# Performance work log

Measured on AMD Instinct MI355X. Metric: run time of the kernel, lower is better.

The kernel has to match this reference:

```python
import jax, jax.numpy as jnp
import numpy as np

MODES = 32
WIDTH = 64
FACTOR = 2
N_LAYERS = 4


def dct_matrix(N):
    # Ortho DCT-II matrix D: dct(x) along last axis = x @ D.T ; idct(y) = y @ D
    n = jnp.arange(N, dtype=jnp.float32)
    k = n[:, None]
    D = jnp.cos(jnp.pi * (n[None, :] + 0.5) * k / N) * jnp.sqrt(2.0 / N)
    D = D.at[0].mul(1.0 / jnp.sqrt(2.0))
    return D


def setup_inputs() -> dict:
    key = jax.random.key(0)
    ks = jax.random.split(key, 16)
    B, M, N, IN_DIM = 4, 256, 256, 12
    hid = WIDTH * FACTOR
    xav_f = jnp.sqrt(2.0 / (WIDTH + WIDTH))  # xavier_normal for (in,out,modes)
    inp = {
        'x': jax.random.normal(ks[0], (B, M, N, IN_DIM), jnp.float32),
        'W_in': jax.random.normal(ks[1], (WIDTH, IN_DIM), jnp.float32) * (1.0 / jnp.sqrt(IN_DIM)),
        'b_in': jnp.zeros((WIDTH,), jnp.float32),
        'fw0': jax.random.normal(ks[2], (N_LAYERS, WIDTH, WIDTH, MODES), jnp.float32) * xav_f,
        'fw1': jax.random.normal(ks[3], (N_LAYERS, WIDTH, WIDTH, MODES), jnp.float32) * xav_f,
        'ffW1': jax.random.normal(ks[4], (N_LAYERS, hid, WIDTH), jnp.float32) * (1.0 / jnp.sqrt(WIDTH)),
        'ffb1': jnp.zeros((N_LAYERS, hid), jnp.float32),
        'ffW2': jax.random.normal(ks[5], (N_LAYERS, WIDTH, hid), jnp.float32) * (1.0 / jnp.sqrt(hid)),
        'ffb2': jnp.zeros((N_LAYERS, WIDTH), jnp.float32),
        'W_o1': jax.random.normal(ks[6], (128, WIDTH), jnp.float32) * (1.0 / jnp.sqrt(WIDTH)),
        'b_o1': jnp.zeros((128,), jnp.float32),
        'W_o2': jax.random.normal(ks[7], (1, 128), jnp.float32) * (1.0 / jnp.sqrt(128.0)),
        'b_o2': jnp.zeros((1,), jnp.float32),
    }
    return inp


def forward_fourier(x, w0, w1, DM, DN):
    # x: [B, M, N, I] channels-last -> [B, I, M, N]
    x = jnp.transpose(x, (0, 3, 1, 2))
    # --- y direction: DCT along N, truncated mode mix, IDCT ---
    x_fty = jnp.einsum('bimn,kn->bimk', x, DN)            # dct, [B,I,M,N]
    xy_m = jnp.einsum('bixy,ioy->boxy', x_fty[..., :MODES], w0)  # [B,O,M,modes]
    xy = jnp.einsum('boxy,yn->boxn', xy_m, DN[:MODES, :])        # idct of zero-padded spectrum
    # --- x direction: DCT along M ---
    x2 = jnp.swapaxes(x, -1, -2)                          # [B,I,N,M]
    x_ftx = jnp.einsum('binm,km->bink', x2, DM)
    xx_m = jnp.einsum('bixy,ioy->boxy', x_ftx[..., :MODES], w1)  # [B,O,N,modes]
    xx = jnp.einsum('boxy,ym->boxm', xx_m, DM[:MODES, :])        # [B,O,N,M]
    xx = jnp.swapaxes(xx, -1, -2)                         # [B,O,M,N]
    out = xx + xy
    return jnp.transpose(out, (0, 2, 3, 1))               # [B,M,N,O]


def feed_forward(h, W1, b1, W2, b2):
    h = jax.nn.relu(h @ W1.T + b1)
    return h @ W2.T + b2


def reference(x, W_in, b_in, fw0, fw1, ffW1, ffb1, ffW2, ffb2, W_o1, b_o1, W_o2, b_o2):
    B, M, N, _ = x.shape
    DM = dct_matrix(M)
    DN = dct_matrix(N)
    x = x @ W_in.T + b_in                                  # in_proj, [B,M,N,width]
    b = x
    for i in range(N_LAYERS):
        h = forward_fourier(x, fw0[i], fw1[i], DM, DN)
        b = feed_forward(h, ffW1[i], ffb1[i], ffW2[i], ffb2[i])
        x = x + b
    # use_fork=False: out applied to the LAST backcast b
    o = jax.nn.relu(b @ W_o1.T + b_o1) * 0 + (b @ W_o1.T + b_o1)  # WNLinear has no activation
    o = b @ W_o1.T + b_o1
    forecast = o @ W_o2.T + b_o2                           # [B,M,N,1]
    return forecast
```

## Files before the change

### kernel.cpp

```cpp
#include <hip/hip_runtime.h>
#include <hip/hip_bf16.h>
#include <math.h>

#define BATCH 4
#define MMDIM 256
#define NNDIM 256
#define CH 64
#define NMODES 32
#define HID 128
#define NLAYERS 4
#define XPLANE 16777216L

typedef __attribute__((ext_vector_type(8))) short bfrag;
typedef __attribute__((ext_vector_type(8))) ushort u16x8;
typedef __attribute__((ext_vector_type(4))) float f32x4;

__device__ inline ushort f2bf(float x) {
    union { float f; uint u; } v; v.f = x;
    uint r = v.u + 0x7fff + ((v.u >> 16) & 1);
    return (ushort)(r >> 16);
}
__device__ inline float bf2f(ushort h) {
    union { uint u; float f; } v; v.u = (uint)h << 16; return v.f;
}
__device__ inline void split(float v, ushort& hi, ushort& lo) {
    __hip_bfloat16 h = __float2bfloat16(v);
    hi = __builtin_bit_cast(ushort, h);
    lo = __builtin_bit_cast(ushort, __float2bfloat16(v - __bfloat162float(h)));
}
#define MFMA __builtin_amdgcn_mfma_f32_16x16x32_bf16


__global__ __launch_bounds__(256) void k_build_T(float* __restrict__ T) {
    int k = blockIdx.x, n = threadIdx.x;
    double v = cos(M_PI * (n + 0.5) * (double)k / 256.0) * sqrt(2.0 / 256.0);
    if (k == 0) v *= 0.7071067811865476;
    T[k * 256 + n] = (float)v;
}

__global__ __launch_bounds__(256) void k_wt(const float* __restrict__ fw, float* __restrict__ wt) {
    int idx = blockIdx.x * 256 + threadIdx.x;
    int l = idx >> 17, r = idx & 131071;
    int y = r >> 12, i = (r >> 6) & 63, o = r & 63;
    wt[idx] = fw[((l * 64 + i) * 64 + o) * 32 + y];
}

__global__ __launch_bounds__(256) void k_Tfrag(const float* __restrict__ T, ushort* __restrict__ Tf) {
    int idx = blockIdx.x * 256 + threadIdx.x;
    int j = idx & 7, lane = (idx >> 3) & 63, ks = (idx >> 9) & 7, yt = idx >> 12;
    float v = T[(yt * 16 + (lane & 15)) * 256 + ks * 32 + ((lane >> 4) << 3) + j];
    ushort hh = f2bf(v);
    Tf[idx] = hh; Tf[idx + 8192] = f2bf(v - bf2f(hh));
}

__global__ __launch_bounds__(256) void k_Ttfrag(const float* __restrict__ T, ushort* __restrict__ Ttf) {
    int idx = blockIdx.x * 256 + threadIdx.x;
    int j = idx & 7, lane = (idx >> 3) & 63, at = idx >> 9;
    float v = T[(((lane >> 4) << 3) + j) * 256 + at * 16 + (lane & 15)];
    ushort hh = f2bf(v);
    Ttf[idx] = hh; Ttf[idx + 8192] = f2bf(v - bf2f(hh));
}

__global__ __launch_bounds__(256) void k_wfrag(const float* __restrict__ W,
                                               ushort* __restrict__ hi, ushort* __restrict__ lo,
                                               int N, int K) {
    int idx = blockIdx.x * 256 + threadIdx.x;
    int per_l = N * K;
    int l = idx / per_l, r = idx % per_l;
    int jj = r & 7, lane = (r >> 3) & 63;
    int ks = (r >> 9) % (K >> 5);
    int nt = r / (512 * (K >> 5));
    int row = nt * 16 + (lane & 15);
    int col = ks * 32 + ((lane >> 4) << 3) + jj;
    float v = W[(long)l * per_l + row * K + col];
    ushort h = f2bf(v);
    hi[idx] = h;
    lo[idx] = f2bf(v - bf2f(h));
}

__global__ void k_head(const float* __restrict__ W_o1, const float* __restrict__ b_o1,
                       const float* __restrict__ W_o2, const float* __restrict__ b_o2,
                       float* __restrict__ Weff, float* __restrict__ beff) {
    int c = threadIdx.x;
    float acc = 0.f;
    for (int j = 0; j < 128; j++) acc += W_o2[j] * W_o1[j * 64 + c];
    Weff[c] = acc;
    if (c == 0) {
        float bb = 0.f;
        for (int j = 0; j < 128; j++) bb += W_o2[j] * b_o1[j];
        beff[0] = bb + b_o2[0];
    }
}

__global__ __launch_bounds__(256) void k_inproj_bf(const float* __restrict__ xin,
                                                   const float* __restrict__ W_in,
                                                   const float* __restrict__ b_in,
                                                   ushort* __restrict__ xbf) {
    __shared__ __align__(16) ushort tile[2][64][72];
    int t = threadIdx.x;
    int bid = blockIdx.x;
    int b = bid >> 10, m = (bid >> 2) & 255, n0 = (bid & 3) * 64;
    int c = t & 63, ng = t >> 6;
    long pbase = (long)(b * 256 + m) * 256 + n0;
    float w[12];
#pragma unroll
    for (int d = 0; d < 12; d++) w[d] = W_in[c * 12 + d];
    float bc = b_in[c];
#pragma unroll 4
    for (int i = 0; i < 16; i++) {
        int nl = ng * 16 + i;
        const float* xr = xin + (pbase + nl) * 12;
        float acc = bc;
#pragma unroll
        for (int d = 0; d < 12; d++) acc += xr[d] * w[d];
        ushort hh, ll;
        split(acc, hh, ll);
        tile[0][c][nl] = hh;
        tile[1][c][nl] = ll;
    }
    __syncthreads();
    int c2 = t >> 2, ch = t & 3;
#pragma unroll
    for (int pl = 0; pl < 2; pl++) {
        const ushort* s = &tile[pl][c2][ch * 16];
        u16x8 v0 = *(const u16x8*)s;
        u16x8 v1 = *(const u16x8*)(s + 8);
        ushort* dst = xbf + (long)pl * XPLANE + ((long)(b * 256 + m) * 64 + c2) * 256 + n0 + ch * 16;
        *(u16x8*)dst = v0; *(u16x8*)(dst + 8) = v1;
    }
}

__global__ __launch_bounds__(256) void k_tx(const ushort* __restrict__ src, ushort* __restrict__ dst) {
    __shared__ __align__(16) ushort tl[64][72];
    int t = threadIdx.x;
    int bid = blockIdx.x;
    int ntile = bid & 3, mt = (bid >> 2) & 3, c = (bid >> 4) & 63, b = (bid >> 10) & 3, pl = bid >> 12;
    int m0 = mt * 64, n0 = ntile * 64;
    const ushort* sp = src + (long)pl * XPLANE;
    ushort* dp = dst + (long)pl * XPLANE;
    {
        int row = t >> 2, ch = (t & 3) * 16;
        const ushort* p = sp + ((long)(b * 256 + m0 + row) * 64 + c) * 256 + n0 + ch;
        u16x8 v0 = *(const u16x8*)p;
        u16x8 v1 = *(const u16x8*)(p + 8);
#pragma unroll
        for (int k = 0; k < 8; k++) tl[ch + k][row] = v0[k];
#pragma unroll
        for (int k = 0; k < 8; k++) tl[ch + 8 + k][row] = v1[k];
    }
    __syncthreads();
    {
        int nrow = t >> 2, mch = (t & 3) * 16;
        const ushort* s = &tl[nrow][mch];
        u16x8 v0 = *(const u16x8*)s;
        u16x8 v1 = *(const u16x8*)(s + 8);
        ushort* p = dp + ((long)(b * 256 + n0 + nrow) * 64 + c) * 256 + m0 + mch;
        *(u16x8*)p = v0; *(u16x8*)(p + 8) = v1;
    }
}

__global__ __launch_bounds__(256) void k_spec(const ushort* __restrict__ xbf,
                                              const ushort* __restrict__ Tf,
                                              const ushort* __restrict__ Ttf,
                                              const float* __restrict__ wt,
                                              float* __restrict__ hdst,
                                              long strideA, long strideF, int accum) {
    __shared__ float Xs[32][68];
    __shared__ __align__(16) ushort Xmb[2][64][40];
    int t = threadIdx.x;
    int lane = t & 63, wv = t >> 6, l15 = lane & 15, l4 = lane >> 4;
    int bf = blockIdx.x;
    const ushort* xb = xbf + (long)bf * 16384;

    f32x4 a0 = {0.f, 0.f, 0.f, 0.f}, a1 = {0.f, 0.f, 0.f, 0.f};
    int c0 = wv * 16;
#pragma unroll
    for (int ks = 0; ks < 8; ks++) {
        const ushort* bp = xb + (c0 + l15) * 256 + ks * 32 + l4 * 8;
        bfrag bhi = *(const bfrag*)bp;
        bfrag blo = *(const bfrag*)(bp + XPLANE);
        const ushort* ap0 = Tf + (long)((0 * 8 + ks) * 64 + lane) * 8;
        const ushort* ap1 = Tf + (long)((1 * 8 + ks) * 64 + lane) * 8;
        bfrag a0h = *(const bfrag*)ap0, a0l = *(const bfrag*)(ap0 + 8192);
        bfrag a1h = *(const bfrag*)ap1, a1l = *(const bfrag*)(ap1 + 8192);
        a0 = MFMA(a0h, bhi, a0, 0, 0, 0);
        a0 = MFMA(a0h, blo, a0, 0, 0, 0);
        a0 = MFMA(a0l, bhi, a0, 0, 0, 0);
        a1 = MFMA(a1h, bhi, a1, 0, 0, 0);
        a1 = MFMA(a1h, blo, a1, 0, 0, 0);
        a1 = MFMA(a1l, bhi, a1, 0, 0, 0);
    }
#pragma unroll
    for (int r = 0; r < 4; r++) {
        Xs[l4 * 4 + r][c0 + l15] = a0[r];
        Xs[16 + l4 * 4 + r][c0 + l15] = a1[r];
    }
    __syncthreads();

    {
        int og = t & 15, yq = t >> 4;
#pragma unroll
        for (int yy = 0; yy < 2; yy++) {
            int y = yq * 2 + yy;
            const float* wb = wt + (long)y * 4096 + og * 4;
            f32x4 a = {0.f, 0.f, 0.f, 0.f};
#pragma unroll 8
            for (int i = 0; i < 64; i++) {
                float xv = Xs[y][i];
                float4 wv = *(const float4*)(wb + i * 64);
                a.x += xv * wv.x; a.y += xv * wv.y; a.z += xv * wv.z; a.w += xv * wv.w;
            }
#pragma unroll
            for (int e = 0; e < 4; e++) {
                ushort hh, ll;
                split(a[e], hh, ll);
                Xmb[0][og * 4 + e][y] = hh;
                Xmb[1][og * 4 + e][y] = ll;
            }
        }
    }
    __syncthreads();

    bfrag vbh[4], vbl[4];
#pragma unroll
    for (int ot = 0; ot < 4; ot++) {
        vbh[ot] = *(const bfrag*)(&Xmb[0][ot * 16 + l15][l4 * 8]);
        vbl[ot] = *(const bfrag*)(&Xmb[1][ot * 16 + l15][l4 * 8]);
    }
    int b = bf >> 8, f = bf & 255;
    float* hb = hdst + (long)b * 4194304 + (long)f * strideF;
#pragma unroll
    for (int ai = 0; ai < 4; ai++) {
        int at = wv * 4 + ai;
        const ushort* ap = Ttf + (long)(at * 64 + lane) * 8;
        bfrag th = *(const bfrag*)ap, tl_ = *(const bfrag*)(ap + 8192);
#pragma unroll
        for (int ot = 0; ot < 4; ot++) {
            f32x4 acc = {0.f, 0.f, 0.f, 0.f};
            acc = MFMA(th, vbh[ot], acc, 0, 0, 0);
            acc = MFMA(th, vbl[ot], acc, 0, 0, 0);
            acc = MFMA(tl_, vbh[ot], acc, 0, 0, 0);
            int arow = at * 16 + l4 * 4;
            float* op = hb + (long)arow * strideA + ot * 16 + l15;
            if (accum) {
#pragma unroll
                for (int r = 0; r < 4; r++) op[(long)r * strideA] += acc[r];
            } else {
#pragma unroll
                for (int r = 0; r < 4; r++) op[(long)r * strideA] = acc[r];
            }
        }
    }
}

#define ASW 136
__global__ __launch_bounds__(256) void k_ff(const float* __restrict__ h,
                                            ushort* __restrict__ xbfw,
                                            const ushort* __restrict__ W1hi, const ushort* __restrict__ W1lo,
                                            const float* __restrict__ b1,
                                            const ushort* __restrict__ W2hi, const ushort* __restrict__ W2lo,
                                            const float* __restrict__ b2,
                                            const float* __restrict__ Weff, const float* __restrict__ beff,
                                            float* __restrict__ out, int last) {
    __shared__ __align__(16) ushort Asb[2][64][ASW];
    int t = threadIdx.x;
    int lane = t & 63, wv = t >> 6;
    int l15 = lane & 15, l4 = lane >> 4;
    long p0 = (long)blockIdx.x * 64;

    f32x4 acc1[8];
#pragma unroll
    for (int nt = 0; nt < 8; nt++) acc1[nt] = (f32x4){0.f, 0.f, 0.f, 0.f};
#pragma unroll
    for (int ks = 0; ks < 2; ks++) {
        const float* hp = h + (p0 + wv * 16 + l15) * 64 + ks * 32 + l4 * 8;
        float4 h0 = *(const float4*)hp;
        float4 h1 = *(const float4*)(hp + 4);
        bfrag ahi, alo;
#pragma unroll
        for (int j = 0; j < 8; j++) {
            float v = (j < 4) ? (&h0.x)[j] : (&h1.x)[j - 4];
            ushort hh, ll;
            split(v, hh, ll);
            ahi[j] = (short)hh; alo[j] = (short)ll;
        }
#pragma unroll
        for (int nt = 0; nt < 8; nt++) {
            long off = (long)((nt * 2 + ks) * 64 + lane) * 8;
            bfrag bhi = *(const bfrag*)(W1hi + off);
            bfrag blo = *(const bfrag*)(W1lo + off);
            acc1[nt] = MFMA(ahi, bhi, acc1[nt], 0, 0, 0);
            acc1[nt] = MFMA(ahi, blo, acc1[nt], 0, 0, 0);
            acc1[nt] = MFMA(alo, bhi, acc1[nt], 0, 0, 0);
        }
    }
#pragma unroll
    for (int nt = 0; nt < 8; nt++) {
        float bj = b1[nt * 16 + l15];
        int j = nt * 16 + l15;
#pragma unroll
        for (int r = 0; r < 4; r++) {
            float v = fmaxf(acc1[nt][r] + bj, 0.f);
            int px = wv * 16 + l4 * 4 + r;
            ushort hh, ll;
            split(v, hh, ll);
            Asb[0][px][j] = hh;
            Asb[1][px][j] = ll;
        }
    }
    __syncthreads();

    f32x4 acc2[4];
#pragma unroll
    for (int nt = 0; nt < 4; nt++) acc2[nt] = (f32x4){0.f, 0.f, 0.f, 0.f};
#pragma unroll
    for (int ks = 0; ks < 4; ks++) {
        bfrag ahi = *(const bfrag*)(&Asb[0][wv * 16 + l15][ks * 32 + l4 * 8]);
        bfrag alo = *(const bfrag*)(&Asb[1][wv * 16 + l15][ks * 32 + l4 * 8]);
#pragma unroll
        for (int nt = 0; nt < 4; nt++) {
            long off = (long)((nt * 4 + ks) * 64 + lane) * 8;
            bfrag bhi = *(const bfrag*)(W2hi + off);
            bfrag blo = *(const bfrag*)(W2lo + off);
            acc2[nt] = MFMA(ahi, bhi, acc2[nt], 0, 0, 0);
            acc2[nt] = MFMA(ahi, blo, acc2[nt], 0, 0, 0);
            acc2[nt] = MFMA(alo, bhi, acc2[nt], 0, 0, 0);
        }
    }

    if (last) {
        float be = beff[0];
#pragma unroll
        for (int r = 0; r < 4; r++) {
            float v = 0.f;
#pragma unroll
            for (int nt = 0; nt < 4; nt++) {
                int c = nt * 16 + l15;
                v += (acc2[nt][r] + b2[c]) * Weff[c];
            }
            v += __shfl_xor(v, 1, 64);
            v += __shfl_xor(v, 2, 64);
            v += __shfl_xor(v, 4, 64);
            v += __shfl_xor(v, 8, 64);
            if (l15 == 0) out[p0 + wv * 16 + l4 * 4 + r] = v + be;
        }
    } else {
        __syncthreads();
        ushort* tile = &Asb[0][0][0];
        int b = (int)(p0 >> 16), m = (int)((p0 >> 8) & 255), n0 = (int)(p0 & 255);
        int c2 = t >> 2, ch = t & 3;
#pragma unroll
        for (int pl = 0; pl < 2; pl++) {
            const ushort* src = xbfw + (long)pl * XPLANE + ((long)(b * 256 + m) * 64 + c2) * 256 + n0 + ch * 16;
            u16x8 v0 = *(const u16x8*)src;
            u16x8 v1 = *(const u16x8*)(src + 8);
            ushort* d = tile + (pl * 64 + c2) * 72 + ch * 16;
            *(u16x8*)d = v0; *(u16x8*)(d + 8) = v1;
        }
        __syncthreads();
#pragma unroll
        for (int nt = 0; nt < 4; nt++) {
            int c = nt * 16 + l15;
            float bc = b2[c];
#pragma unroll
            for (int r = 0; r < 4; r++) {
                int nl = wv * 16 + l4 * 4 + r;
                float res = bf2f(tile[(0 * 64 + c) * 72 + nl]) + bf2f(tile[(1 * 64 + c) * 72 + nl]);
                float v = res + acc2[nt][r] + bc;
                ushort hh, ll;
                split(v, hh, ll);
                tile[(0 * 64 + c) * 72 + nl] = hh;
                tile[(1 * 64 + c) * 72 + nl] = ll;
            }
        }
        __syncthreads();
#pragma unroll
        for (int pl = 0; pl < 2; pl++) {
            const ushort* s = tile + (pl * 64 + c2) * 72 + ch * 16;
            u16x8 v0 = *(const u16x8*)s;
            u16x8 v1 = *(const u16x8*)(s + 8);
            ushort* dst = xbfw + (long)pl * XPLANE + ((long)(b * 256 + m) * 64 + c2) * 256 + n0 + ch * 16;
            *(u16x8*)dst = v0; *(u16x8*)(dst + 8) = v1;
        }
    }
}


extern "C" void kernel_launch(void* const* d_in, const int* in_sizes, int n_in,
                              void* d_out, int out_size, void* d_ws, size_t ws_size,
                              hipStream_t stream) {
    const float* x_in = (const float*)d_in[0];
    const float* W_in = (const float*)d_in[1];
    const float* b_in = (const float*)d_in[2];
    const float* fw0  = (const float*)d_in[3];
    const float* fw1  = (const float*)d_in[4];
    const float* ffW1 = (const float*)d_in[5];
    const float* ffb1 = (const float*)d_in[6];
    const float* ffW2 = (const float*)d_in[7];
    const float* ffb2 = (const float*)d_in[8];
    const float* W_o1 = (const float*)d_in[9];
    const float* b_o1 = (const float*)d_in[10];
    const float* W_o2 = (const float*)d_in[11];
    const float* b_o2 = (const float*)d_in[12];
    float* out = (float*)d_out;

    float* ws   = (float*)d_ws;
    float* T    = ws;
    float* w0t  = T + 8192;
    float* w1t  = w0t + 524288;
    float* Weff = w1t + 524288;
    float* beff = Weff + 64;
    float* h    = beff + 64;
    ushort* Tfrag  = (ushort*)(h + 16777216);
    ushort* Ttfrag = Tfrag + 16384;
    ushort* W1f_hi = Ttfrag + 16384;
    ushort* W1f_lo = W1f_hi + 32768;
    ushort* W2f_hi = W1f_lo + 32768;
    ushort* W2f_lo = W2f_hi + 32768;
    ushort* xbf_y  = W2f_lo + 32768;
    ushort* xbf_x  = xbf_y + 2 * XPLANE;

    k_build_T<<<32, 256, 0, stream>>>(T);
    k_wt<<<2048, 256, 0, stream>>>(fw0, w0t);
    k_wt<<<2048, 256, 0, stream>>>(fw1, w1t);
    k_Tfrag<<<32, 256, 0, stream>>>(T, Tfrag);
    k_Ttfrag<<<32, 256, 0, stream>>>(T, Ttfrag);
    k_wfrag<<<(NLAYERS * HID * CH) / 256, 256, 0, stream>>>(ffW1, W1f_hi, W1f_lo, HID, CH);
    k_wfrag<<<(NLAYERS * CH * HID) / 256, 256, 0, stream>>>(ffW2, W2f_hi, W2f_lo, CH, HID);
    k_head<<<1, 64, 0, stream>>>(W_o1, b_o1, W_o2, b_o2, Weff, beff);
    k_inproj_bf<<<4096, 256, 0, stream>>>(x_in, W_in, b_in, xbf_y);

    for (int l = 0; l < NLAYERS; l++) {
        k_spec<<<1024, 256, 0, stream>>>(xbf_y, Tfrag, Ttfrag, w0t + (long)l * 131072,
                                         h, 64L, 16384L, 0);
        k_tx<<<8192, 256, 0, stream>>>(xbf_y, xbf_x);
        k_spec<<<1024, 256, 0, stream>>>(xbf_x, Tfrag, Ttfrag, w1t + (long)l * 131072,
                                         h, 16384L, 64L, 1);
        k_ff<<<4096, 256, 0, stream>>>(h, xbf_y,
            W1f_hi + (long)l * HID * CH, W1f_lo + (long)l * HID * CH,
            ffb1 + (long)l * HID,
            W2f_hi + (long)l * CH * HID, W2f_lo + (long)l * CH * HID,
            ffb2 + (long)l * CH,
            Weff, beff, out, (l == NLAYERS - 1) ? 1 : 0);
    }
}
```

Baseline: 725.9 us.

## Pair spectral slices per block, prefetch FF residual, fuse setup kernels

```diff
diff --git a/kernel.cpp b/kernel.cpp
--- a/kernel.cpp
+++ b/kernel.cpp
@@ -31,34 +31,38 @@
 #define MFMA __builtin_amdgcn_mfma_f32_16x16x32_bf16
 
 
-__global__ __launch_bounds__(256) void k_build_T(float* __restrict__ T) {
-    int k = blockIdx.x, n = threadIdx.x;
-    double v = cos(M_PI * (n + 0.5) * (double)k / 256.0) * sqrt(2.0 / 256.0);
-    if (k == 0) v *= 0.7071067811865476;
-    T[k * 256 + n] = (float)v;
-}
-
-__global__ __launch_bounds__(256) void k_wt(const float* __restrict__ fw, float* __restrict__ wt) {
-    int idx = blockIdx.x * 256 + threadIdx.x;
-    int l = idx >> 17, r = idx & 131071;
-    int y = r >> 12, i = (r >> 6) & 63, o = r & 63;
-    wt[idx] = fw[((l * 64 + i) * 64 + o) * 32 + y];
-}
-
-__global__ __launch_bounds__(256) void k_Tfrag(const float* __restrict__ T, ushort* __restrict__ Tf) {
+__global__ __launch_bounds__(256) void k_Tfrag(ushort* __restrict__ Tf) {
     int idx = blockIdx.x * 256 + threadIdx.x;
     int j = idx & 7, lane = (idx >> 3) & 63, ks = (idx >> 9) & 7, yt = idx >> 12;
-    float v = T[(yt * 16 + (lane & 15)) * 256 + ks * 32 + ((lane >> 4) << 3) + j];
-    ushort hh = f2bf(v);
-    Tf[idx] = hh; Tf[idx + 8192] = f2bf(v - bf2f(hh));
-}
-
-__global__ __launch_bounds__(256) void k_Ttfrag(const float* __restrict__ T, ushort* __restrict__ Ttf) {
+    int k = yt * 16 + (lane & 15);
+    int n = ks * 32 + ((lane >> 4) << 3) + j;
+    double v = cos(M_PI * (n + 0.5) * (double)k / 256.0) * 0.08838834764831845;
+    if (k == 0) v *= 0.7071067811865476;
+    float vf = (float)v;
+    ushort hh = f2bf(vf);
+    Tf[idx] = hh; Tf[idx + 8192] = f2bf(vf - bf2f(hh));
+}
+
+__global__ __launch_bounds__(256) void k_Ttfrag(ushort* __restrict__ Ttf) {
     int idx = blockIdx.x * 256 + threadIdx.x;
     int j = idx & 7, lane = (idx >> 3) & 63, at = idx >> 9;
-    float v = T[(((lane >> 4) << 3) + j) * 256 + at * 16 + (lane & 15)];
-    ushort hh = f2bf(v);
-    Ttf[idx] = hh; Ttf[idx + 8192] = f2bf(v - bf2f(hh));
+    int k = ((lane >> 4) << 3) + j;
+    int n = at * 16 + (lane & 15);
+    double v = cos(M_PI * (n + 0.5) * (double)k / 256.0) * 0.08838834764831845;
+    if (k == 0) v *= 0.7071067811865476;
+    float vf = (float)v;
+    ushort hh = f2bf(vf);
+    Ttf[idx] = hh; Ttf[idx + 8192] = f2bf(vf - bf2f(hh));
+}
+
+__global__ __launch_bounds__(256) void k_wt(const float* __restrict__ fw0, const float* __restrict__ fw1,
+                                            float* __restrict__ wt01) {
+    int idx = blockIdx.x * 256 + threadIdx.x;
+    const float* fw = (idx < 524288) ? fw0 : fw1;
+    int i2 = idx & 524287;
+    int l = i2 >> 17, r = i2 & 131071;
+    int y = r >> 12, i = (r >> 6) & 63, o = r & 63;
+    wt01[idx] = fw[((l * 64 + i) * 64 + o) * 32 + y];
 }
 
 __global__ __launch_bounds__(256) void k_wfrag(const float* __restrict__ W,
@@ -159,64 +163,68 @@
     }
 }
 
-__global__ __launch_bounds__(256) void k_spec(const ushort* __restrict__ xbf,
+__global__ __launch_bounds__(512) void k_spec(const ushort* __restrict__ xbf,
                                               const ushort* __restrict__ Tf,
                                               const ushort* __restrict__ Ttf,
                                               const float* __restrict__ wt,
                                               float* __restrict__ hdst,
                                               long strideA, long strideF, int accum) {
-    __shared__ float Xs[32][68];
-    __shared__ __align__(16) ushort Xmb[2][64][40];
+    __shared__ float Xs[2][32][68];
+    __shared__ __align__(16) ushort Xmb[2][2][64][40];
     int t = threadIdx.x;
     int lane = t & 63, wv = t >> 6, l15 = lane & 15, l4 = lane >> 4;
-    int bf = blockIdx.x;
-    const ushort* xb = xbf + (long)bf * 16384;
-
-    f32x4 a0 = {0.f, 0.f, 0.f, 0.f}, a1 = {0.f, 0.f, 0.f, 0.f};
-    int c0 = wv * 16;
-#pragma unroll
-    for (int ks = 0; ks < 8; ks++) {
-        const ushort* bp = xb + (c0 + l15) * 256 + ks * 32 + l4 * 8;
-        bfrag bhi = *(const bfrag*)bp;
-        bfrag blo = *(const bfrag*)(bp + XPLANE);
-        const ushort* ap0 = Tf + (long)((0 * 8 + ks) * 64 + lane) * 8;
-        const ushort* ap1 = Tf + (long)((1 * 8 + ks) * 64 + lane) * 8;
-        bfrag a0h = *(const bfrag*)ap0, a0l = *(const bfrag*)(ap0 + 8192);
-        bfrag a1h = *(const bfrag*)ap1, a1l = *(const bfrag*)(ap1 + 8192);
-        a0 = MFMA(a0h, bhi, a0, 0, 0, 0);
-        a0 = MFMA(a0h, blo, a0, 0, 0, 0);
-        a0 = MFMA(a0l, bhi, a0, 0, 0, 0);
-        a1 = MFMA(a1h, bhi, a1, 0, 0, 0);
-        a1 = MFMA(a1h, blo, a1, 0, 0, 0);
-        a1 = MFMA(a1l, bhi, a1, 0, 0, 0);
-    }
-#pragma unroll
-    for (int r = 0; r < 4; r++) {
-        Xs[l4 * 4 + r][c0 + l15] = a0[r];
-        Xs[16 + l4 * 4 + r][c0 + l15] = a1[r];
+    int fp = blockIdx.x & 127, b = blockIdx.x >> 7;
+    int s_ = wv >> 2;
+
+    {
+        const ushort* xb = xbf + ((long)(b * 256 + fp * 2 + s_)) * 16384;
+        f32x4 a0 = {0.f, 0.f, 0.f, 0.f}, a1 = {0.f, 0.f, 0.f, 0.f};
+        int c0 = (wv & 3) * 16;
+#pragma unroll
+        for (int ks = 0; ks < 8; ks++) {
+            const ushort* bp = xb + (c0 + l15) * 256 + ks * 32 + l4 * 8;
+            bfrag bhi = *(const bfrag*)bp;
+            bfrag blo = *(const bfrag*)(bp + XPLANE);
+            const ushort* ap0 = Tf + (long)((0 * 8 + ks) * 64 + lane) * 8;
+            const ushort* ap1 = Tf + (long)((1 * 8 + ks) * 64 + lane) * 8;
+            bfrag a0h = *(const bfrag*)ap0, a0l = *(const bfrag*)(ap0 + 8192);
+            bfrag a1h = *(const bfrag*)ap1, a1l = *(const bfrag*)(ap1 + 8192);
+            a0 = MFMA(a0h, bhi, a0, 0, 0, 0);
+            a0 = MFMA(a0h, blo, a0, 0, 0, 0);
+            a0 = MFMA(a0l, bhi, a0, 0, 0, 0);
+            a1 = MFMA(a1h, bhi, a1, 0, 0, 0);
+            a1 = MFMA(a1h, blo, a1, 0, 0, 0);
+            a1 = MFMA(a1l, bhi, a1, 0, 0, 0);
+        }
+#pragma unroll
+        for (int r = 0; r < 4; r++) {
+            Xs[s_][l4 * 4 + r][c0 + l15] = a0[r];
+            Xs[s_][16 + l4 * 4 + r][c0 + l15] = a1[r];
+        }
     }
     __syncthreads();
 
     {
-        int og = t & 15, yq = t >> 4;
-#pragma unroll
-        for (int yy = 0; yy < 2; yy++) {
-            int y = yq * 2 + yy;
-            const float* wb = wt + (long)y * 4096 + og * 4;
-            f32x4 a = {0.f, 0.f, 0.f, 0.f};
+        int og = t & 15, y = t >> 4;
+        const float* wb = wt + (long)y * 4096 + og * 4;
+        f32x4 A0 = {0.f, 0.f, 0.f, 0.f}, A1 = {0.f, 0.f, 0.f, 0.f};
 #pragma unroll 8
-            for (int i = 0; i < 64; i++) {
-                float xv = Xs[y][i];
-                float4 wv = *(const float4*)(wb + i * 64);
-                a.x += xv * wv.x; a.y += xv * wv.y; a.z += xv * wv.z; a.w += xv * wv.w;
-            }
-#pragma unroll
-            for (int e = 0; e < 4; e++) {
-                ushort hh, ll;
-                split(a[e], hh, ll);
-                Xmb[0][og * 4 + e][y] = hh;
-                Xmb[1][og * 4 + e][y] = ll;
-            }
+        for (int i = 0; i < 64; i++) {
+            float4 wv4 = *(const float4*)(wb + i * 64);
+            float x0 = Xs[0][y][i];
+            float x1 = Xs[1][y][i];
+            A0.x += x0 * wv4.x; A0.y += x0 * wv4.y; A0.z += x0 * wv4.z; A0.w += x0 * wv4.w;
+            A1.x += x1 * wv4.x; A1.y += x1 * wv4.y; A1.z += x1 * wv4.z; A1.w += x1 * wv4.w;
+        }
+#pragma unroll
+        for (int e = 0; e < 4; e++) {
+            ushort hh, ll;
+            split(A0[e], hh, ll);
+            Xmb[0][0][og * 4 + e][y] = hh;
+            Xmb[0][1][og * 4 + e][y] = ll;
+            split(A1[e], hh, ll);
+            Xmb[1][0][og * 4 + e][y] = hh;
+            Xmb[1][1][og * 4 + e][y] = ll;
         }
     }
     __syncthreads();
@@ -224,14 +232,14 @@
     bfrag vbh[4], vbl[4];
 #pragma unroll
     for (int ot = 0; ot < 4; ot++) {
-        vbh[ot] = *(const bfrag*)(&Xmb[0][ot * 16 + l15][l4 * 8]);
-        vbl[ot] = *(const bfrag*)(&Xmb[1][ot * 16 + l15][l4 * 8]);
-    }
-    int b = bf >> 8, f = bf & 255;
+        vbh[ot] = *(const bfrag*)(&Xmb[s_][0][ot * 16 + l15][l4 * 8]);
+        vbl[ot] = *(const bfrag*)(&Xmb[s_][1][ot * 16 + l15][l4 * 8]);
+    }
+    int f = fp * 2 + s_;
     float* hb = hdst + (long)b * 4194304 + (long)f * strideF;
 #pragma unroll
     for (int ai = 0; ai < 4; ai++) {
-        int at = wv * 4 + ai;
+        int at = (wv & 3) * 4 + ai;
         const ushort* ap = Ttf + (long)(at * 64 + lane) * 8;
         bfrag th = *(const bfrag*)ap, tl_ = *(const bfrag*)(ap + 8192);
 #pragma unroll
@@ -267,33 +275,50 @@
     int lane = t & 63, wv = t >> 6;
     int l15 = lane & 15, l4 = lane >> 4;
     long p0 = (long)blockIdx.x * 64;
+    int b = (int)(p0 >> 16), m = (int)((p0 >> 8) & 255), n0 = (int)(p0 & 255);
+    int c2 = t >> 2, ch = t & 3;
+
+    u16x8 r0a, r0b, r1a, r1b;
+    if (!last) {
+        const ushort* src0 = xbfw + ((long)(b * 256 + m) * 64 + c2) * 256 + n0 + ch * 16;
+        r0a = *(const u16x8*)src0;
+        r0b = *(const u16x8*)(src0 + 8);
+        r1a = *(const u16x8*)(src0 + XPLANE);
+        r1b = *(const u16x8*)(src0 + XPLANE + 8);
+    }
 
     f32x4 acc1[8];
 #pragma unroll
     for (int nt = 0; nt < 8; nt++) acc1[nt] = (f32x4){0.f, 0.f, 0.f, 0.f};
+    bfrag ahi_[2], alo_[2];
 #pragma unroll
     for (int ks = 0; ks < 2; ks++) {
         const float* hp = h + (p0 + wv * 16 + l15) * 64 + ks * 32 + l4 * 8;
         float4 h0 = *(const float4*)hp;
         float4 h1 = *(const float4*)(hp + 4);
-        bfrag ahi, alo;
 #pragma unroll
         for (int j = 0; j < 8; j++) {
             float v = (j < 4) ? (&h0.x)[j] : (&h1.x)[j - 4];
             ushort hh, ll;
             split(v, hh, ll);
-            ahi[j] = (short)hh; alo[j] = (short)ll;
-        }
+            ahi_[ks][j] = (short)hh; alo_[ks][j] = (short)ll;
+        }
+    }
+#pragma unroll
+    for (int ks = 0; ks < 2; ks++)
 #pragma unroll
         for (int nt = 0; nt < 8; nt++) {
-            long off = (long)((nt * 2 + ks) * 64 + lane) * 8;
-            bfrag bhi = *(const bfrag*)(W1hi + off);
-            bfrag blo = *(const bfrag*)(W1lo + off);
-            acc1[nt] = MFMA(ahi, bhi, acc1[nt], 0, 0, 0);
-            acc1[nt] = MFMA(ahi, blo, acc1[nt], 0, 0, 0);
-            acc1[nt] = MFMA(alo, bhi, acc1[nt], 0, 0, 0);
-        }
-    }
+            bfrag bhi = *(const bfrag*)(W1hi + (long)((nt * 2 + ks) * 64 + lane) * 8);
+            acc1[nt] = MFMA(ahi_[ks], bhi, acc1[nt], 0, 0, 0);
+            acc1[nt] = MFMA(alo_[ks], bhi, acc1[nt], 0, 0, 0);
+        }
+#pragma unroll
+    for (int ks = 0; ks < 2; ks++)
+#pragma unroll
+        for (int nt = 0; nt < 8; nt++) {
+            bfrag blo = *(const bfrag*)(W1lo + (long)((nt * 2 + ks) * 64 + lane) * 8);
+            acc1[nt] = MFMA(ahi_[ks], blo, acc1[nt], 0, 0, 0);
+        }
 #pragma unroll
     for (int nt = 0; nt < 8; nt++) {
         float bj = b1[nt * 16 + l15];
@@ -319,12 +344,18 @@
         bfrag alo = *(const bfrag*)(&Asb[1][wv * 16 + l15][ks * 32 + l4 * 8]);
 #pragma unroll
         for (int nt = 0; nt < 4; nt++) {
-            long off = (long)((nt * 4 + ks) * 64 + lane) * 8;
-            bfrag bhi = *(const bfrag*)(W2hi + off);
-            bfrag blo = *(const bfrag*)(W2lo + off);
+            bfrag bhi = *(const bfrag*)(W2hi + (long)((nt * 4 + ks) * 64 + lane) * 8);
             acc2[nt] = MFMA(ahi, bhi, acc2[nt], 0, 0, 0);
+            acc2[nt] = MFMA(alo, bhi, acc2[nt], 0, 0, 0);
+        }
+    }
+#pragma unroll
+    for (int ks = 0; ks < 4; ks++) {
+        bfrag ahi = *(const bfrag*)(&Asb[0][wv * 16 + l15][ks * 32 + l4 * 8]);
+#pragma unroll
+        for (int nt = 0; nt < 4; nt++) {
+            bfrag blo = *(const bfrag*)(W2lo + (long)((nt * 4 + ks) * 64 + lane) * 8);
             acc2[nt] = MFMA(ahi, blo, acc2[nt], 0, 0, 0);
-            acc2[nt] = MFMA(alo, bhi, acc2[nt], 0, 0, 0);
         }
     }
 
@@ -346,18 +377,7 @@
         }
     } else {
         __syncthreads();
-        ushort* tile = &Asb[0][0][0];
-        int b = (int)(p0 >> 16), m = (int)((p0 >> 8) & 255), n0 = (int)(p0 & 255);
-        int c2 = t >> 2, ch = t & 3;
-#pragma unroll
-        for (int pl = 0; pl < 2; pl++) {
-            const ushort* src = xbfw + (long)pl * XPLANE + ((long)(b * 256 + m) * 64 + c2) * 256 + n0 + ch * 16;
-            u16x8 v0 = *(const u16x8*)src;
-            u16x8 v1 = *(const u16x8*)(src + 8);
-            ushort* d = tile + (pl * 64 + c2) * 72 + ch * 16;
-            *(u16x8*)d = v0; *(u16x8*)(d + 8) = v1;
-        }
-        __syncthreads();
+        float* dt = (float*)(&Asb[0][0][0]);
 #pragma unroll
         for (int nt = 0; nt < 4; nt++) {
             int c = nt * 16 + l15;
@@ -365,23 +385,25 @@
 #pragma unroll
             for (int r = 0; r < 4; r++) {
                 int nl = wv * 16 + l4 * 4 + r;
-                float res = bf2f(tile[(0 * 64 + c) * 72 + nl]) + bf2f(tile[(1 * 64 + c) * 72 + nl]);
-                float v = res + acc2[nt][r] + bc;
-                ushort hh, ll;
-                split(v, hh, ll);
-                tile[(0 * 64 + c) * 72 + nl] = hh;
-                tile[(1 * 64 + c) * 72 + nl] = ll;
+                dt[c * 69 + nl] = acc2[nt][r] + bc;
             }
         }
         __syncthreads();
-#pragma unroll
-        for (int pl = 0; pl < 2; pl++) {
-            const ushort* s = tile + (pl * 64 + c2) * 72 + ch * 16;
-            u16x8 v0 = *(const u16x8*)s;
-            u16x8 v1 = *(const u16x8*)(s + 8);
-            ushort* dst = xbfw + (long)pl * XPLANE + ((long)(b * 256 + m) * 64 + c2) * 256 + n0 + ch * 16;
-            *(u16x8*)dst = v0; *(u16x8*)(dst + 8) = v1;
-        }
+        const float* drow = dt + c2 * 69 + ch * 16;
+        ushort oh[16], ol[16];
+#pragma unroll
+        for (int k = 0; k < 16; k++) {
+            ushort rh = (k < 8) ? r0a[k] : r0b[k - 8];
+            ushort rl = (k < 8) ? r1a[k] : r1b[k - 8];
+            float v = bf2f(rh) + bf2f(rl) + drow[k];
+            split(v, oh[k], ol[k]);
+        }
+        ushort* dst = xbfw + ((long)(b * 256 + m) * 64 + c2) * 256 + n0 + ch * 16;
+        u16x8 w0, w1, w2, w3;
+#pragma unroll
+        for (int k = 0; k < 8; k++) { w0[k] = oh[k]; w1[k] = oh[k + 8]; w2[k] = ol[k]; w3[k] = ol[k + 8]; }
+        *(u16x8*)dst = w0; *(u16x8*)(dst + 8) = w1;
+        *(u16x8*)(dst + XPLANE) = w2; *(u16x8*)(dst + XPLANE + 8) = w3;
     }
 }
 
@@ -405,8 +427,7 @@
     float* out = (float*)d_out;
 
     float* ws   = (float*)d_ws;
-    float* T    = ws;
-    float* w0t  = T + 8192;
+    float* w0t  = ws;
     float* w1t  = w0t + 524288;
     float* Weff = w1t + 524288;
     float* beff = Weff + 64;
@@ -420,22 +441,20 @@
     ushort* xbf_y  = W2f_lo + 32768;
     ushort* xbf_x  = xbf_y + 2 * XPLANE;
 
-    k_build_T<<<32, 256, 0, stream>>>(T);
-    k_wt<<<2048, 256, 0, stream>>>(fw0, w0t);
-    k_wt<<<2048, 256, 0, stream>>>(fw1, w1t);
-    k_Tfrag<<<32, 256, 0, stream>>>(T, Tfrag);
-    k_Ttfrag<<<32, 256, 0, stream>>>(T, Ttfrag);
+    k_Tfrag<<<32, 256, 0, stream>>>(Tfrag);
+    k_Ttfrag<<<32, 256, 0, stream>>>(Ttfrag);
+    k_wt<<<4096, 256, 0, stream>>>(fw0, fw1, w0t);
     k_wfrag<<<(NLAYERS * HID * CH) / 256, 256, 0, stream>>>(ffW1, W1f_hi, W1f_lo, HID, CH);
     k_wfrag<<<(NLAYERS * CH * HID) / 256, 256, 0, stream>>>(ffW2, W2f_hi, W2f_lo, CH, HID);
     k_head<<<1, 64, 0, stream>>>(W_o1, b_o1, W_o2, b_o2, Weff, beff);
     k_inproj_bf<<<4096, 256, 0, stream>>>(x_in, W_in, b_in, xbf_y);
 
     for (int l = 0; l < NLAYERS; l++) {
-        k_spec<<<1024, 256, 0, stream>>>(xbf_y, Tfrag, Ttfrag, w0t + (long)l * 131072,
-                                         h, 64L, 16384L, 0);
+        k_spec<<<512, 512, 0, stream>>>(xbf_y, Tfrag, Ttfrag, w0t + (long)l * 131072,
+                                        h, 64L, 16384L, 0);
         k_tx<<<8192, 256, 0, stream>>>(xbf_y, xbf_x);
-        k_spec<<<1024, 256, 0, stream>>>(xbf_x, Tfrag, Ttfrag, w1t + (long)l * 131072,
-                                         h, 16384L, 64L, 1);
+        k_spec<<<512, 512, 0, stream>>>(xbf_x, Tfrag, Ttfrag, w1t + (long)l * 131072,
+                                        h, 16384L, 64L, 1);
         k_ff<<<4096, 256, 0, stream>>>(h, xbf_y,
             W1f_hi + (long)l * HID * CH, W1f_lo + (long)l * HID * CH,
             ffb1 + (long)l * HID,
```

Result: slower. 835.6 us (+15.1%).
